# Kernel tuning notes

Hardware: AMD Instinct MI355X
Metric: run time of the kernel (lower is better)

The kernel has to match this reference:

```python
import jax, jax.numpy as jnp
import numpy as np

N = 100000
E = 1_600_000
IN_CH = 64
HID = 32       # per-head hidden dim
HEADS = 4
OUT_CH = 6
NEG_SLOPE = 0.2


def _glorot(key, shape):
    fan_in, fan_out = shape[0], shape[-1]
    lim = jnp.sqrt(6.0 / (fan_in + fan_out))
    return jax.random.uniform(key, shape, jnp.float32, -lim, lim)


def setup_inputs() -> dict:
    key = jax.random.key(0)
    ks = jax.random.split(key, 20)
    x = jax.random.normal(ks[0], (N, IN_CH), jnp.float32)
    edge_index = jax.random.randint(ks[1], (2, E), 0, N, jnp.int64)
    batch = jnp.zeros((N,), jnp.int64)
    inp = {"x": x, "edge_index": edge_index, "batch": batch}
    inp["W0"] = _glorot(ks[2], (IN_CH, HEADS * HID))
    inp["as0"] = _glorot(ks[3], (HEADS, HID))
    inp["ad0"] = _glorot(ks[4], (HEADS, HID))
    inp["b0"] = jnp.zeros((HEADS * HID,), jnp.float32)
    inp["W1"] = _glorot(ks[5], (HEADS * HID, HEADS * HID))
    inp["as1"] = _glorot(ks[6], (HEADS, HID))
    inp["ad1"] = _glorot(ks[7], (HEADS, HID))
    inp["b1"] = jnp.zeros((HEADS * HID,), jnp.float32)
    inp["W2"] = _glorot(ks[8], (HEADS * HID, HEADS * HID))
    inp["as2"] = _glorot(ks[9], (HEADS, HID))
    inp["ad2"] = _glorot(ks[10], (HEADS, HID))
    inp["b2"] = jnp.zeros((HEADS * HID,), jnp.float32)
    # final layer: 128 -> 6, 1 head, no concat (mean)
    inp["W3"] = _glorot(ks[11], (HEADS * HID, OUT_CH))
    inp["as3"] = _glorot(ks[12], (1, OUT_CH))
    inp["ad3"] = _glorot(ks[13], (1, OUT_CH))
    inp["b3"] = jnp.zeros((OUT_CH,), jnp.float32)
    return inp


def gat_conv(x, src, dst, W, a_src, a_dst, b, heads, concat):
    """PyG GATConv: linear -> per-edge attention -> segment softmax over dst -> scatter-add."""
    n = x.shape[0]
    h = (x @ W).reshape(n, heads, -1)                       # [N,H,D]
    al_s = jnp.sum(h * a_src, axis=-1)                      # [N,H]
    al_d = jnp.sum(h * a_dst, axis=-1)                      # [N,H]
    e = jax.nn.leaky_relu(al_s[src] + al_d[dst], NEG_SLOPE)  # [E,H]
    m = jax.ops.segment_max(e, dst, num_segments=n)         # segment softmax (stable)
    ex = jnp.exp(e - m[dst])
    s = jax.ops.segment_sum(ex, dst, num_segments=n)
    alpha = ex / (s[dst] + 1e-16)                           # [E,H]
    out = jax.ops.segment_sum(alpha[:, :, None] * h[src], dst, num_segments=n)  # [N,H,D]
    out = out.reshape(n, -1) if concat else out.mean(axis=1)
    return out + b


def reference(x, edge_index, batch, W0, as0, ad0, b0, W1, as1, ad1, b1,
              W2, as2, ad2, b2, W3, as3, ad3, b3):
    n = x.shape[0]
    # PyG GATConv adds self-loops by default; edge set is static (no pooling), add once.
    ar = jnp.arange(n, dtype=edge_index.dtype)
    ei = jnp.concatenate([edge_index, jnp.stack([ar, ar])], axis=1)
    src, dst = ei[0], ei[1]
    x = jax.nn.elu(gat_conv(x, src, dst, W0, as0, ad0, b0, HEADS, True))
    x = jax.nn.elu(gat_conv(x, src, dst, W1, as1, ad1, b1, HEADS, True))
    x = jax.nn.elu(gat_conv(x, src, dst, W2, as2, ad2, b2, HEADS, True))
    x = gat_conv(x, src, dst, W3, as3, ad3, b3, 1, False)   # final layer: no activation
    return x
```

## Files before the change

### kernel.cpp

```cpp
#include <hip/hip_runtime.h>
#include <hip/hip_bf16.h>
#include <hip/hip_fp16.h>

#define IN_CH 64
#define HID 32
#define HEADS 4
#define OUT_CH 6
#define NEG_SLOPE 0.2f

typedef __attribute__((ext_vector_type(8))) _Float16 half8;
typedef __attribute__((ext_vector_type(4))) float f32x4;


#define PBLK 256
#define CAP 6144

__global__ __launch_bounds__(256) void part_count(const int* __restrict__ ei, int E, int EN,
                                                  int NB, int epb, int* __restrict__ counts) {
    __shared__ int cnt[512];
    int b = blockIdx.x, t = threadIdx.x;
    for (int i = t; i < NB; i += 256) cnt[i] = 0;
    __syncthreads();
    int e0 = b * epb;
    int e1 = min(e0 + epb, EN);
    for (int e = e0 + t; e < e1; e += 256) {
        int d = (e < E) ? ei[E + e] : (e - E);
        atomicAdd(&cnt[d >> 8], 1);
    }
    __syncthreads();
    for (int i = t; i < NB; i += 256) counts[(size_t)i * PBLK + b] = cnt[i];
}

__global__ __launch_bounds__(256) void bucket_tot(const int* __restrict__ counts,
                                                  int* __restrict__ btot) {
    __shared__ int red[256];
    int k = blockIdx.x, t = threadIdx.x;
    red[t] = counts[(size_t)k * PBLK + t];
    __syncthreads();
    for (int off = 128; off; off >>= 1) {
        if (t < off) red[t] += red[t + off];
        __syncthreads();
    }
    if (t == 0) btot[k] = red[0];
}

__global__ __launch_bounds__(256) void bucket_scan(const int* __restrict__ btot, int NB, int EN,
                                                   int* __restrict__ bstart) {
    __shared__ int tmp[256];
    int t = threadIdx.x;
    int chunk = (NB + 255) >> 8;
    int s0 = t * chunk, s1 = min(s0 + chunk, NB);
    int sum = 0;
    for (int i = s0; i < s1; ++i) sum += btot[i];
    tmp[t] = sum;
    __syncthreads();
    for (int off = 1; off < 256; off <<= 1) {
        int v = (t >= off) ? tmp[t - off] : 0;
        __syncthreads();
        tmp[t] += v;
        __syncthreads();
    }
    int run = (t == 0) ? 0 : tmp[t - 1];
    for (int i = s0; i < s1; ++i) {
        int c = btot[i];
        bstart[i] = run;
        run += c;
    }
    if (t == 255) bstart[NB] = EN;
}

__global__ __launch_bounds__(256) void bucket_base(int* __restrict__ counts,
                                                   const int* __restrict__ bstart) {
    __shared__ int sc[256];
    int k = blockIdx.x, t = threadIdx.x;
    int v = counts[(size_t)k * PBLK + t];
    sc[t] = v;
    __syncthreads();
    for (int off = 1; off < 256; off <<= 1) {
        int u = (t >= off) ? sc[t - off] : 0;
        __syncthreads();
        sc[t] += u;
        __syncthreads();
    }
    counts[(size_t)k * PBLK + t] = bstart[k] + sc[t] - v;
}

__global__ __launch_bounds__(256) void part_scatter(const int* __restrict__ ei, int E, int EN,
                                                    int NB, int epb,
                                                    const int* __restrict__ base,
                                                    int2* __restrict__ ebuf) {
    __shared__ int cur[512];
    int b = blockIdx.x, t = threadIdx.x;
    for (int i = t; i < NB; i += 256) cur[i] = base[(size_t)i * PBLK + b];
    __syncthreads();
    int e0 = b * epb;
    int e1 = min(e0 + epb, EN);
    for (int e = e0 + t; e < e1; e += 256) {
        int s, d;
        if (e < E) { s = ei[e]; d = ei[E + e]; }
        else       { s = e - E; d = s; }
        int slot = atomicAdd(&cur[d >> 8], 1);
        ebuf[slot] = make_int2(s, d & 255);
    }
}

__global__ __launch_bounds__(256) void bucket_csr(const int2* __restrict__ ebuf,
                                                  const int* __restrict__ bstart,
                                                  int NB, int N, int EN,
                                                  int* __restrict__ row_start,
                                                  int* __restrict__ csr_src) {
    __shared__ int cnt[256];
    __shared__ int sc[256];
    __shared__ int stage[CAP];
    int k = blockIdx.x, t = threadIdx.x;
    int s0 = bstart[k], s1 = bstart[k + 1];
    int len = s1 - s0;
    cnt[t] = 0;
    __syncthreads();
    for (int i = t; i < len; i += 256) atomicAdd(&cnt[ebuf[s0 + i].y], 1);
    __syncthreads();
    int v = cnt[t];
    sc[t] = v;
    __syncthreads();
    for (int off = 1; off < 256; off <<= 1) {
        int u = (t >= off) ? sc[t - off] : 0;
        __syncthreads();
        sc[t] += u;
        __syncthreads();
    }
    int excl = sc[t] - v;
    int g = (k << 8) + t;
    if (g < N) row_start[g] = s0 + excl;
    if (k == NB - 1 && t == 0) row_start[N] = EN;
    bool fits = (len <= CAP);
    cnt[t] = fits ? excl : s0 + excl;
    __syncthreads();
    if (fits) {
        for (int i = t; i < len; i += 256) {
            int2 e = ebuf[s0 + i];
            int slot = atomicAdd(&cnt[e.y], 1);
            stage[slot] = e.x;
        }
        __syncthreads();
        for (int i = t; i < len; i += 256) csr_src[s0 + i] = stage[i];
    } else {
        for (int i = t; i < len; i += 256) {
            int2 e = ebuf[s0 + i];
            int slot = atomicAdd(&cnt[e.y], 1);
            csr_src[slot] = e.x;
        }
    }
}


__global__ void xconv_kernel(const float* __restrict__ x, __half* __restrict__ xh, int total4) {
    int t = blockIdx.x * blockDim.x + threadIdx.x;
    if (t >= total4) return;
    float4 v = *reinterpret_cast<const float4*>(x + (size_t)t * 4);
    __half2* op = reinterpret_cast<__half2*>(xh + (size_t)t * 4);
    op[0] = __float22half2_rn(make_float2(v.x, v.y));
    op[1] = __float22half2_rn(make_float2(v.z, v.w));
}

__global__ void wtrans_kernel(const float* __restrict__ W, __half* __restrict__ WT,
                              int K, int kshift) {
    int o = blockIdx.x * blockDim.x + threadIdx.x;
    if (o >= (K << 7)) return;
    int c = o >> kshift;
    int k = o & (K - 1);
    WT[o] = __float2half(W[(size_t)k * 128 + c]);
}


__global__ __launch_bounds__(256) void gemm_mfma(const __half* __restrict__ A,
                                                 const __half* __restrict__ WT,
                                                 const float* __restrict__ avs,
                                                 const float* __restrict__ avd,
                                                 __half* __restrict__ C,
                                                 float* __restrict__ als,
                                                 float* __restrict__ ald,
                                                 int N, int K) {
    int tid = threadIdx.x;
    int wv = tid >> 6, lane = tid & 63;
    int row0 = blockIdx.x * 64 + wv * 16;
    int lrow = lane & 15;
    int lk = (lane >> 4) * 8;
    int garow = row0 + lrow;

    half8 afrag[4];
#pragma unroll
    for (int ks = 0; ks < 4; ++ks) {
        half8 z = {(_Float16)0, (_Float16)0, (_Float16)0, (_Float16)0,
                   (_Float16)0, (_Float16)0, (_Float16)0, (_Float16)0};
        afrag[ks] = z;
    }
    if (garow < N) {
        const __half* ap = A + (size_t)garow * K + lk;
        if (K == 128) {
#pragma unroll
            for (int ks = 0; ks < 4; ++ks)
                afrag[ks] = *reinterpret_cast<const half8*>(ap + ks * 32);
        } else {
#pragma unroll
            for (int ks = 0; ks < 2; ++ks)
                afrag[ks] = *reinterpret_cast<const half8*>(ap + ks * 32);
        }
    }

    f32x4 acc[8];
#pragma unroll
    for (int t = 0; t < 8; ++t) acc[t] = (f32x4){0.f, 0.f, 0.f, 0.f};

#pragma unroll
    for (int t = 0; t < 8; ++t) {
        const __half* wb = WT + (size_t)(t * 16 + lrow) * K + lk;
        if (K == 128) {
#pragma unroll
            for (int ks = 0; ks < 4; ++ks) {
                half8 bfrag = *reinterpret_cast<const half8*>(wb + ks * 32);
                acc[t] = __builtin_amdgcn_mfma_f32_16x16x32_f16(afrag[ks], bfrag, acc[t], 0, 0, 0);
            }
        } else {
#pragma unroll
            for (int ks = 0; ks < 2; ++ks) {
                half8 bfrag = *reinterpret_cast<const half8*>(wb + ks * 32);
                acc[t] = __builtin_amdgcn_mfma_f32_16x16x32_f16(afrag[ks], bfrag, acc[t], 0, 0, 0);
            }
        }
    }

    int rbase = (lane >> 4) * 4;
#pragma unroll
    for (int t = 0; t < 8; ++t) {
#pragma unroll
        for (int j = 0; j < 4; ++j) {
            int gr = row0 + rbase + j;
            if (gr < N) C[(size_t)gr * 128 + t * 16 + lrow] = __float2half(acc[t][j]);
        }
    }
    float ps[4][4], pd[4][4];
#pragma unroll
    for (int h = 0; h < 4; ++h)
#pragma unroll
        for (int j = 0; j < 4; ++j) { ps[h][j] = 0.f; pd[h][j] = 0.f; }
#pragma unroll
    for (int t = 0; t < 8; ++t) {
        int ht = t >> 1;
        float as_c = avs[t * 16 + lrow];
        float ad_c = avd[t * 16 + lrow];
#pragma unroll
        for (int j = 0; j < 4; ++j) {
            ps[ht][j] += acc[t][j] * as_c;
            pd[ht][j] += acc[t][j] * ad_c;
        }
    }
#pragma unroll
    for (int h = 0; h < 4; ++h) {
#pragma unroll
        for (int j = 0; j < 4; ++j) {
            float s = ps[h][j], d = pd[h][j];
            s += __shfl_xor(s, 1); d += __shfl_xor(d, 1);
            s += __shfl_xor(s, 2); d += __shfl_xor(d, 2);
            s += __shfl_xor(s, 4); d += __shfl_xor(d, 4);
            s += __shfl_xor(s, 8); d += __shfl_xor(d, 8);
            if (lrow == 0) {
                int gr = row0 + rbase + j;
                if (gr < N) {
                    als[(size_t)gr * 4 + h] = s;
                    ald[(size_t)gr * 4 + h] = d;
                }
            }
        }
    }
}


__device__ __forceinline__ float lrelu(float x) { return x > 0.f ? x : NEG_SLOPE * x; }

__global__ __launch_bounds__(256) void agg_kernel(const __half* __restrict__ h,
                                                  const float* __restrict__ als4,
                                                  const float* __restrict__ ald4,
                                                  const int* __restrict__ row_start,
                                                  const int* __restrict__ csr_src,
                                                  const float* __restrict__ bias,
                                                  __half* __restrict__ xout,
                                                  int N, int applyElu) {
    int v = (int)((blockIdx.x * blockDim.x + threadIdx.x) >> 6);
    int lane = threadIdx.x & 63;
    if (v >= N) return;
    int base = row_start[v], end = row_start[v + 1];

    int half_ = lane >> 5;
    int dim4 = (lane & 31) * 4;
    int hd2  = (lane & 31) >> 3;

    float aldh = ald4[(size_t)v * 4 + hd2];
    float alsh = als4[(size_t)v * 4 + hd2];
    float em = lrelu(alsh + aldh);
    const __half* hdim = h + dim4;
    const float* alsb = als4 + hd2;

    float4 acc  = make_float4(0.f, 0.f, 0.f, 0.f);
    float4 acc2 = make_float4(0.f, 0.f, 0.f, 0.f);
    float ssum = 0.f, ssum2 = 0.f;

    int j = base + half_;
    for (; j + 6 < end; j += 8) {
        int s0 = csr_src[j + 0];
        int s1 = csr_src[j + 2];
        int s2 = csr_src[j + 4];
        int s3 = csr_src[j + 6];
        float a0 = alsb[(size_t)s0 * 4];
        float a1 = alsb[(size_t)s1 * 4];
        float a2 = alsb[(size_t)s2 * 4];
        float a3 = alsb[(size_t)s3 * 4];
        uint2 r0 = *reinterpret_cast<const uint2*>(hdim + (size_t)s0 * 128);
        uint2 r1 = *reinterpret_cast<const uint2*>(hdim + (size_t)s1 * 128);
        uint2 r2 = *reinterpret_cast<const uint2*>(hdim + (size_t)s2 * 128);
        uint2 r3 = *reinterpret_cast<const uint2*>(hdim + (size_t)s3 * 128);
        float e0 = __expf(lrelu(a0 + aldh) - em);
        float e1 = __expf(lrelu(a1 + aldh) - em);
        float e2 = __expf(lrelu(a2 + aldh) - em);
        float e3 = __expf(lrelu(a3 + aldh) - em);
        ssum  += e0 + e2;
        ssum2 += e1 + e3;
        float2 f0a = __half22float2(*reinterpret_cast<__half2*>(&r0.x));
        float2 f0b = __half22float2(*reinterpret_cast<__half2*>(&r0.y));
        float2 f1a = __half22float2(*reinterpret_cast<__half2*>(&r1.x));
        float2 f1b = __half22float2(*reinterpret_cast<__half2*>(&r1.y));
        float2 f2a = __half22float2(*reinterpret_cast<__half2*>(&r2.x));
        float2 f2b = __half22float2(*reinterpret_cast<__half2*>(&r2.y));
        float2 f3a = __half22float2(*reinterpret_cast<__half2*>(&r3.x));
        float2 f3b = __half22float2(*reinterpret_cast<__half2*>(&r3.y));
        acc.x  += e0 * f0a.x; acc.y  += e0 * f0a.y; acc.z  += e0 * f0b.x; acc.w  += e0 * f0b.y;
        acc2.x += e1 * f1a.x; acc2.y += e1 * f1a.y; acc2.z += e1 * f1b.x; acc2.w += e1 * f1b.y;
        acc.x  += e2 * f2a.x; acc.y  += e2 * f2a.y; acc.z  += e2 * f2b.x; acc.w  += e2 * f2b.y;
        acc2.x += e3 * f3a.x; acc2.y += e3 * f3a.y; acc2.z += e3 * f3b.x; acc2.w += e3 * f3b.y;
    }
    for (; j < end; j += 2) {
        int s0 = csr_src[j];
        float a0 = alsb[(size_t)s0 * 4];
        uint2 r0 = *reinterpret_cast<const uint2*>(hdim + (size_t)s0 * 128);
        float e0 = __expf(lrelu(a0 + aldh) - em);
        ssum += e0;
        float2 f0a = __half22float2(*reinterpret_cast<__half2*>(&r0.x));
        float2 f0b = __half22float2(*reinterpret_cast<__half2*>(&r0.y));
        acc.x += e0 * f0a.x; acc.y += e0 * f0a.y; acc.z += e0 * f0b.x; acc.w += e0 * f0b.y;
    }
    acc.x += acc2.x; acc.y += acc2.y; acc.z += acc2.z; acc.w += acc2.w;
    ssum += ssum2;
    acc.x += __shfl_xor(acc.x, 32);
    acc.y += __shfl_xor(acc.y, 32);
    acc.z += __shfl_xor(acc.z, 32);
    acc.w += __shfl_xor(acc.w, 32);
    ssum  += __shfl_xor(ssum, 32);

    if (lane < 32) {
        float inv = 1.0f / (ssum + 1e-16f);
        float4 bv = *reinterpret_cast<const float4*>(bias + dim4);
        float4 o;
        o.x = acc.x * inv + bv.x;
        o.y = acc.y * inv + bv.y;
        o.z = acc.z * inv + bv.z;
        o.w = acc.w * inv + bv.w;
        if (applyElu) {
            o.x = o.x > 0.f ? o.x : expm1f(o.x);
            o.y = o.y > 0.f ? o.y : expm1f(o.y);
            o.z = o.z > 0.f ? o.z : expm1f(o.z);
            o.w = o.w > 0.f ? o.w : expm1f(o.w);
        }
        __half2* op = reinterpret_cast<__half2*>(xout + (size_t)v * 128 + dim4);
        op[0] = __float22half2_rn(make_float2(o.x, o.y));
        op[1] = __float22half2_rn(make_float2(o.z, o.w));
    }
}


__global__ void gemm3_kernel(const __half* __restrict__ x, const float* __restrict__ W,
                             const float* __restrict__ as3, const float* __restrict__ ad3,
                             float* __restrict__ h3, float* __restrict__ als3,
                             float* __restrict__ ald3, int N) {
    int n = blockIdx.x * blockDim.x + threadIdx.x;
    if (n >= N) return;
    float acc[6] = {0.f, 0.f, 0.f, 0.f, 0.f, 0.f};
    const __half* xp = x + (size_t)n * 128;
#pragma unroll 2
    for (int k8 = 0; k8 < 16; ++k8) {
        uint4 rv = *reinterpret_cast<const uint4*>(xp + k8 * 8);
        float2 fa = __half22float2(*reinterpret_cast<__half2*>(&rv.x));
        float2 fb = __half22float2(*reinterpret_cast<__half2*>(&rv.y));
        float2 fc = __half22float2(*reinterpret_cast<__half2*>(&rv.z));
        float2 fd = __half22float2(*reinterpret_cast<__half2*>(&rv.w));
        float xv[8] = {fa.x, fa.y, fb.x, fb.y, fc.x, fc.y, fd.x, fd.y};
        const float* w0 = W + (size_t)(k8 * 8) * 6;
#pragma unroll
        for (int kk = 0; kk < 8; ++kk)
#pragma unroll
            for (int q = 0; q < 6; ++q)
                acc[q] += xv[kk] * w0[kk * 6 + q];
    }
    float s = 0.f, d = 0.f;
#pragma unroll
    for (int q = 0; q < 6; ++q) {
        s += acc[q] * as3[q];
        d += acc[q] * ad3[q];
        h3[(size_t)n * 6 + q] = acc[q];
    }
    als3[n] = s;
    ald3[n] = d;
}

__global__ void agg3_kernel(const float* __restrict__ h3, const float* __restrict__ als3,
                            const float* __restrict__ ald3, const int* __restrict__ row_start,
                            const int* __restrict__ csr_src, const float* __restrict__ b3,
                            float* __restrict__ out, int N) {
    int v = blockIdx.x * blockDim.x + threadIdx.x;
    if (v >= N) return;
    int base = row_start[v], end = row_start[v + 1];
    float aldv = ald3[v];
    float em = lrelu(als3[v] + aldv);
    float ssum = 0.f;
    float acc[6] = {0.f, 0.f, 0.f, 0.f, 0.f, 0.f};
    float acc2[6] = {0.f, 0.f, 0.f, 0.f, 0.f, 0.f};
    int j = base;
    for (; j + 1 < end; j += 2) {
        int sa = csr_src[j], sb = csr_src[j + 1];
        float ea = __expf(lrelu(als3[sa] + aldv) - em);
        float eb = __expf(lrelu(als3[sb] + aldv) - em);
        ssum += ea + eb;
        const float* ha = h3 + (size_t)sa * 6;
        const float* hb = h3 + (size_t)sb * 6;
#pragma unroll
        for (int q = 0; q < 6; ++q) acc[q] += ea * ha[q];
#pragma unroll
        for (int q = 0; q < 6; ++q) acc2[q] += eb * hb[q];
    }
    if (j < end) {
        int sa = csr_src[j];
        float ea = __expf(lrelu(als3[sa] + aldv) - em);
        ssum += ea;
        const float* ha = h3 + (size_t)sa * 6;
#pragma unroll
        for (int q = 0; q < 6; ++q) acc[q] += ea * ha[q];
    }
    float inv = 1.f / (ssum + 1e-16f);
#pragma unroll
    for (int q = 0; q < 6; ++q) out[(size_t)v * 6 + q] = (acc[q] + acc2[q]) * inv + b3[q];
}


extern "C" void kernel_launch(void* const* d_in, const int* in_sizes, int n_in,
                              void* d_out, int out_size, void* d_ws, size_t ws_size,
                              hipStream_t stream) {
    const float* x    = (const float*)d_in[0];
    const int*   ei   = (const int*)d_in[1];
    const float* W0   = (const float*)d_in[3];
    const float* as0  = (const float*)d_in[4];
    const float* ad0  = (const float*)d_in[5];
    const float* b0   = (const float*)d_in[6];
    const float* W1   = (const float*)d_in[7];
    const float* as1  = (const float*)d_in[8];
    const float* ad1  = (const float*)d_in[9];
    const float* b1   = (const float*)d_in[10];
    const float* W2   = (const float*)d_in[11];
    const float* as2  = (const float*)d_in[12];
    const float* ad2  = (const float*)d_in[13];
    const float* b2   = (const float*)d_in[14];
    const float* W3   = (const float*)d_in[15];
    const float* as3  = (const float*)d_in[16];
    const float* ad3  = (const float*)d_in[17];
    const float* b3   = (const float*)d_in[18];
    float* out = (float*)d_out;

    int N = in_sizes[0] / IN_CH;
    int E = in_sizes[1] / 2;
    int EN = E + N;
    int NB = (N + 255) >> 8;
    int epb = (EN + PBLK - 1) / PBLK;

    char* p = (char*)d_ws;
    auto alloc = [&](size_t bytes) {
        char* q = p;
        p += (bytes + 255) & ~(size_t)255;
        return q;
    };
    __half* xh   = (__half*)alloc((size_t)N * 64 * 2);
    __half* hbuf = (__half*)alloc((size_t)N * 128 * 2);
    __half* xA   = (__half*)alloc((size_t)N * 128 * 2);
    __half* xB   = (__half*)alloc((size_t)N * 128 * 2);
    __half* WT0  = (__half*)alloc((size_t)128 * 64 * 2);
    __half* WT1  = (__half*)alloc((size_t)128 * 128 * 2);
    __half* WT2  = (__half*)alloc((size_t)128 * 128 * 2);
    float* als  = (float*)alloc((size_t)N * 4 * 4);
    float* ald  = (float*)alloc((size_t)N * 4 * 4);
    float* h3   = (float*)alloc((size_t)N * 6 * 4);
    float* als3 = (float*)alloc((size_t)N * 4);
    float* ald3 = (float*)alloc((size_t)N * 4);
    int* row_start = (int*)alloc((size_t)(N + 1) * 4);
    int* csr_src   = (int*)alloc((size_t)EN * 4);
    int2* ebuf     = (int2*)alloc((size_t)EN * 8);
    int* counts    = (int*)alloc((size_t)NB * PBLK * 4);
    int* btot      = (int*)alloc((size_t)NB * 4);
    int* bstart    = (int*)alloc((size_t)(NB + 1) * 4);
    (void)ws_size; (void)n_in; (void)out_size;

    part_count<<<PBLK, 256, 0, stream>>>(ei, E, EN, NB, epb, counts);
    bucket_tot<<<NB, 256, 0, stream>>>(counts, btot);
    bucket_scan<<<1, 256, 0, stream>>>(btot, NB, EN, bstart);
    bucket_base<<<NB, 256, 0, stream>>>(counts, bstart);
    part_scatter<<<PBLK, 256, 0, stream>>>(ei, E, EN, NB, epb, counts, ebuf);
    bucket_csr<<<NB, 256, 0, stream>>>(ebuf, bstart, NB, N, EN, row_start, csr_src);

    xconv_kernel<<<(N * 16 + 255) / 256, 256, 0, stream>>>(x, xh, N * 16);
    wtrans_kernel<<<(128 * 64 + 255) / 256, 256, 0, stream>>>(W0, WT0, 64, 6);
    wtrans_kernel<<<(128 * 128 + 255) / 256, 256, 0, stream>>>(W1, WT1, 128, 7);
    wtrans_kernel<<<(128 * 128 + 255) / 256, 256, 0, stream>>>(W2, WT2, 128, 7);

    int gemm_grid = (N + 63) / 64;
    int agg_grid  = (N + 3) / 4;
    int n_grid    = (N + 255) / 256;

    gemm_mfma<<<gemm_grid, 256, 0, stream>>>(xh, WT0, as0, ad0, hbuf, als, ald, N, 64);
    agg_kernel<<<agg_grid, 256, 0, stream>>>(hbuf, als, ald, row_start, csr_src, b0, xA, N, 1);

    gemm_mfma<<<gemm_grid, 256, 0, stream>>>(xA, WT1, as1, ad1, hbuf, als, ald, N, 128);
    agg_kernel<<<agg_grid, 256, 0, stream>>>(hbuf, als, ald, row_start, csr_src, b1, xB, N, 1);

    gemm_mfma<<<gemm_grid, 256, 0, stream>>>(xB, WT2, as2, ad2, hbuf, als, ald, N, 128);
    agg_kernel<<<agg_grid, 256, 0, stream>>>(hbuf, als, ald, row_start, csr_src, b2, xA, N, 1);

    gemm3_kernel<<<n_grid, 256, 0, stream>>>(xA, W3, as3, ad3, h3, als3, ald3, N);
    agg3_kernel<<<n_grid, 256, 0, stream>>>(h3, als3, ald3, row_start, csr_src, b3, out, N);
}
```

Measured before the change: 445.8 us.

## Compute edge softmax weights once per chunk in LDS; fuse input fp16 conversion into GEMM

The aggregation kernel now processes each node's edges in chunks of 64. In each chunk every lane loads one source index and all four heads' attention logits as a float4, computes the four exp weights and stages them with the source index in shared memory. The gather loop then reads those staged values, so the redundant per-head exp and logit loads that each lane group used to repeat are removed. The first-layer GEMM now reads the fp32 input directly and converts it in registers, which eliminates the separate xconv pass and its buffer. The staging adds LDS traffic and wave barriers per chunk, and the half-to-float conversions now go through unions.

```diff
diff --git a/kernel.cpp b/kernel.cpp
--- a/kernel.cpp
+++ b/kernel.cpp
@@ -153,15 +153,6 @@
 }
 
 
-__global__ void xconv_kernel(const float* __restrict__ x, __half* __restrict__ xh, int total4) {
-    int t = blockIdx.x * blockDim.x + threadIdx.x;
-    if (t >= total4) return;
-    float4 v = *reinterpret_cast<const float4*>(x + (size_t)t * 4);
-    __half2* op = reinterpret_cast<__half2*>(xh + (size_t)t * 4);
-    op[0] = __float22half2_rn(make_float2(v.x, v.y));
-    op[1] = __float22half2_rn(make_float2(v.z, v.w));
-}
-
 __global__ void wtrans_kernel(const float* __restrict__ W, __half* __restrict__ WT,
                               int K, int kshift) {
     int o = blockIdx.x * blockDim.x + threadIdx.x;
@@ -173,6 +164,7 @@
 
 
 __global__ __launch_bounds__(256) void gemm_mfma(const __half* __restrict__ A,
+                                                 const float* __restrict__ Af,
                                                  const __half* __restrict__ WT,
                                                  const float* __restrict__ avs,
                                                  const float* __restrict__ avd,
@@ -195,15 +187,21 @@
         afrag[ks] = z;
     }
     if (garow < N) {
-        const __half* ap = A + (size_t)garow * K + lk;
         if (K == 128) {
+            const __half* ap = A + (size_t)garow * 128 + lk;
 #pragma unroll
             for (int ks = 0; ks < 4; ++ks)
                 afrag[ks] = *reinterpret_cast<const half8*>(ap + ks * 32);
         } else {
-#pragma unroll
-            for (int ks = 0; ks < 2; ++ks)
-                afrag[ks] = *reinterpret_cast<const half8*>(ap + ks * 32);
+            const float* ap = Af + (size_t)garow * 64 + lk;
+#pragma unroll
+            for (int ks = 0; ks < 2; ++ks) {
+                float4 f0 = *reinterpret_cast<const float4*>(ap + ks * 32);
+                float4 f1 = *reinterpret_cast<const float4*>(ap + ks * 32 + 4);
+                half8 fr = {(_Float16)f0.x, (_Float16)f0.y, (_Float16)f0.z, (_Float16)f0.w,
+                            (_Float16)f1.x, (_Float16)f1.y, (_Float16)f1.z, (_Float16)f1.w};
+                afrag[ks] = fr;
+            }
         }
     }
 
@@ -285,7 +283,10 @@
                                                   const float* __restrict__ bias,
                                                   __half* __restrict__ xout,
                                                   int N, int applyElu) {
-    int v = (int)((blockIdx.x * blockDim.x + threadIdx.x) >> 6);
+    __shared__ float ex_s[4][256];
+    __shared__ int   so_s[4][64];
+    int w = threadIdx.x >> 6;
+    int v = blockIdx.x * 4 + w;
     int lane = threadIdx.x & 63;
     if (v >= N) return;
     int base = row_start[v], end = row_start[v + 1];
@@ -294,68 +295,83 @@
     int dim4 = (lane & 31) * 4;
     int hd2  = (lane & 31) >> 3;
 
-    float aldh = ald4[(size_t)v * 4 + hd2];
-    float alsh = als4[(size_t)v * 4 + hd2];
-    float em = lrelu(alsh + aldh);
+    float4 aldv = *reinterpret_cast<const float4*>(ald4 + (size_t)v * 4);
+    float4 alsv = *reinterpret_cast<const float4*>(als4 + (size_t)v * 4);
+    float4 em4;
+    em4.x = lrelu(alsv.x + aldv.x);
+    em4.y = lrelu(alsv.y + aldv.y);
+    em4.z = lrelu(alsv.z + aldv.z);
+    em4.w = lrelu(alsv.w + aldv.w);
+
     const __half* hdim = h + dim4;
-    const float* alsb = als4 + hd2;
-
+    float4 sum4 = make_float4(0.f, 0.f, 0.f, 0.f);
     float4 acc  = make_float4(0.f, 0.f, 0.f, 0.f);
     float4 acc2 = make_float4(0.f, 0.f, 0.f, 0.f);
-    float ssum = 0.f, ssum2 = 0.f;
-
-    int j = base + half_;
-    for (; j + 6 < end; j += 8) {
-        int s0 = csr_src[j + 0];
-        int s1 = csr_src[j + 2];
-        int s2 = csr_src[j + 4];
-        int s3 = csr_src[j + 6];
-        float a0 = alsb[(size_t)s0 * 4];
-        float a1 = alsb[(size_t)s1 * 4];
-        float a2 = alsb[(size_t)s2 * 4];
-        float a3 = alsb[(size_t)s3 * 4];
-        uint2 r0 = *reinterpret_cast<const uint2*>(hdim + (size_t)s0 * 128);
-        uint2 r1 = *reinterpret_cast<const uint2*>(hdim + (size_t)s1 * 128);
-        uint2 r2 = *reinterpret_cast<const uint2*>(hdim + (size_t)s2 * 128);
-        uint2 r3 = *reinterpret_cast<const uint2*>(hdim + (size_t)s3 * 128);
-        float e0 = __expf(lrelu(a0 + aldh) - em);
-        float e1 = __expf(lrelu(a1 + aldh) - em);
-        float e2 = __expf(lrelu(a2 + aldh) - em);
-        float e3 = __expf(lrelu(a3 + aldh) - em);
-        ssum  += e0 + e2;
-        ssum2 += e1 + e3;
-        float2 f0a = __half22float2(*reinterpret_cast<__half2*>(&r0.x));
-        float2 f0b = __half22float2(*reinterpret_cast<__half2*>(&r0.y));
-        float2 f1a = __half22float2(*reinterpret_cast<__half2*>(&r1.x));
-        float2 f1b = __half22float2(*reinterpret_cast<__half2*>(&r1.y));
-        float2 f2a = __half22float2(*reinterpret_cast<__half2*>(&r2.x));
-        float2 f2b = __half22float2(*reinterpret_cast<__half2*>(&r2.y));
-        float2 f3a = __half22float2(*reinterpret_cast<__half2*>(&r3.x));
-        float2 f3b = __half22float2(*reinterpret_cast<__half2*>(&r3.y));
-        acc.x  += e0 * f0a.x; acc.y  += e0 * f0a.y; acc.z  += e0 * f0b.x; acc.w  += e0 * f0b.y;
-        acc2.x += e1 * f1a.x; acc2.y += e1 * f1a.y; acc2.z += e1 * f1b.x; acc2.w += e1 * f1b.y;
-        acc.x  += e2 * f2a.x; acc.y  += e2 * f2a.y; acc.z  += e2 * f2b.x; acc.w  += e2 * f2b.y;
-        acc2.x += e3 * f3a.x; acc2.y += e3 * f3a.y; acc2.z += e3 * f3b.x; acc2.w += e3 * f3b.y;
-    }
-    for (; j < end; j += 2) {
-        int s0 = csr_src[j];
-        float a0 = alsb[(size_t)s0 * 4];
-        uint2 r0 = *reinterpret_cast<const uint2*>(hdim + (size_t)s0 * 128);
-        float e0 = __expf(lrelu(a0 + aldh) - em);
-        ssum += e0;
-        float2 f0a = __half22float2(*reinterpret_cast<__half2*>(&r0.x));
-        float2 f0b = __half22float2(*reinterpret_cast<__half2*>(&r0.y));
-        acc.x += e0 * f0a.x; acc.y += e0 * f0a.y; acc.z += e0 * f0b.x; acc.w += e0 * f0b.y;
+
+    for (int c = base; c < end; c += 64) {
+        int j = c + lane;
+        bool valid = j < end;
+        int s = valid ? csr_src[j] : 0;
+        float4 ex4 = make_float4(0.f, 0.f, 0.f, 0.f);
+        if (valid) {
+            float4 a = *reinterpret_cast<const float4*>(als4 + (size_t)s * 4);
+            ex4.x = __expf(lrelu(a.x + aldv.x) - em4.x);
+            ex4.y = __expf(lrelu(a.y + aldv.y) - em4.y);
+            ex4.z = __expf(lrelu(a.z + aldv.z) - em4.z);
+            ex4.w = __expf(lrelu(a.w + aldv.w) - em4.w);
+            sum4.x += ex4.x; sum4.y += ex4.y; sum4.z += ex4.z; sum4.w += ex4.w;
+        }
+        *reinterpret_cast<float4*>(&ex_s[w][lane * 4]) = ex4;
+        so_s[w][lane] = s;
+        __builtin_amdgcn_wave_barrier();
+        asm volatile("" ::: "memory");
+
+        int cnt = end - c; if (cnt > 64) cnt = 64;
+        int t = half_;
+        for (; t + 6 < cnt; t += 8) {
+            int i0 = t, i1 = t + 2, i2 = t + 4, i3 = t + 6;
+            int s0 = so_s[w][i0], s1 = so_s[w][i1], s2 = so_s[w][i2], s3 = so_s[w][i3];
+            float e0 = ex_s[w][i0 * 4 + hd2], e1 = ex_s[w][i1 * 4 + hd2];
+            float e2 = ex_s[w][i2 * 4 + hd2], e3 = ex_s[w][i3 * 4 + hd2];
+            union { uint2 u; __half hh[4]; } r0, r1, r2, r3;
+            r0.u = *reinterpret_cast<const uint2*>(hdim + (size_t)s0 * 128);
+            r1.u = *reinterpret_cast<const uint2*>(hdim + (size_t)s1 * 128);
+            r2.u = *reinterpret_cast<const uint2*>(hdim + (size_t)s2 * 128);
+            r3.u = *reinterpret_cast<const uint2*>(hdim + (size_t)s3 * 128);
+            acc.x  += e0 * (float)r0.hh[0]; acc.y  += e0 * (float)r0.hh[1];
+            acc.z  += e0 * (float)r0.hh[2]; acc.w  += e0 * (float)r0.hh[3];
+            acc2.x += e1 * (float)r1.hh[0]; acc2.y += e1 * (float)r1.hh[1];
+            acc2.z += e1 * (float)r1.hh[2]; acc2.w += e1 * (float)r1.hh[3];
+            acc.x  += e2 * (float)r2.hh[0]; acc.y  += e2 * (float)r2.hh[1];
+            acc.z  += e2 * (float)r2.hh[2]; acc.w  += e2 * (float)r2.hh[3];
+            acc2.x += e3 * (float)r3.hh[0]; acc2.y += e3 * (float)r3.hh[1];
+            acc2.z += e3 * (float)r3.hh[2]; acc2.w += e3 * (float)r3.hh[3];
+        }
+        for (; t < cnt; t += 2) {
+            int s0 = so_s[w][t];
+            float e0 = ex_s[w][t * 4 + hd2];
+            union { uint2 u; __half hh[4]; } r0;
+            r0.u = *reinterpret_cast<const uint2*>(hdim + (size_t)s0 * 128);
+            acc.x += e0 * (float)r0.hh[0]; acc.y += e0 * (float)r0.hh[1];
+            acc.z += e0 * (float)r0.hh[2]; acc.w += e0 * (float)r0.hh[3];
+        }
+        __builtin_amdgcn_wave_barrier();
+        asm volatile("" ::: "memory");
     }
     acc.x += acc2.x; acc.y += acc2.y; acc.z += acc2.z; acc.w += acc2.w;
-    ssum += ssum2;
     acc.x += __shfl_xor(acc.x, 32);
     acc.y += __shfl_xor(acc.y, 32);
     acc.z += __shfl_xor(acc.z, 32);
     acc.w += __shfl_xor(acc.w, 32);
-    ssum  += __shfl_xor(ssum, 32);
-
+#pragma unroll
+    for (int off = 32; off; off >>= 1) {
+        sum4.x += __shfl_xor(sum4.x, off);
+        sum4.y += __shfl_xor(sum4.y, off);
+        sum4.z += __shfl_xor(sum4.z, off);
+        sum4.w += __shfl_xor(sum4.w, off);
+    }
     if (lane < 32) {
+        float ssum = (hd2 == 0) ? sum4.x : (hd2 == 1) ? sum4.y : (hd2 == 2) ? sum4.z : sum4.w;
         float inv = 1.0f / (ssum + 1e-16f);
         float4 bv = *reinterpret_cast<const float4*>(bias + dim4);
         float4 o;
@@ -386,18 +402,16 @@
     const __half* xp = x + (size_t)n * 128;
 #pragma unroll 2
     for (int k8 = 0; k8 < 16; ++k8) {
-        uint4 rv = *reinterpret_cast<const uint4*>(xp + k8 * 8);
-        float2 fa = __half22float2(*reinterpret_cast<__half2*>(&rv.x));
-        float2 fb = __half22float2(*reinterpret_cast<__half2*>(&rv.y));
-        float2 fc = __half22float2(*reinterpret_cast<__half2*>(&rv.z));
-        float2 fd = __half22float2(*reinterpret_cast<__half2*>(&rv.w));
-        float xv[8] = {fa.x, fa.y, fb.x, fb.y, fc.x, fc.y, fd.x, fd.y};
+        union { uint4 u; __half hh[8]; } rv;
+        rv.u = *reinterpret_cast<const uint4*>(xp + k8 * 8);
         const float* w0 = W + (size_t)(k8 * 8) * 6;
 #pragma unroll
-        for (int kk = 0; kk < 8; ++kk)
+        for (int kk = 0; kk < 8; ++kk) {
+            float xv = (float)rv.hh[kk];
 #pragma unroll
             for (int q = 0; q < 6; ++q)
-                acc[q] += xv[kk] * w0[kk * 6 + q];
+                acc[q] += xv * w0[kk * 6 + q];
+        }
     }
     float s = 0.f, d = 0.f;
 #pragma unroll
@@ -484,7 +498,6 @@
         p += (bytes + 255) & ~(size_t)255;
         return q;
     };
-    __half* xh   = (__half*)alloc((size_t)N * 64 * 2);
     __half* hbuf = (__half*)alloc((size_t)N * 128 * 2);
     __half* xA   = (__half*)alloc((size_t)N * 128 * 2);
     __half* xB   = (__half*)alloc((size_t)N * 128 * 2);
@@ -511,7 +524,6 @@
     part_scatter<<<PBLK, 256, 0, stream>>>(ei, E, EN, NB, epb, counts, ebuf);
     bucket_csr<<<NB, 256, 0, stream>>>(ebuf, bstart, NB, N, EN, row_start, csr_src);
 
-    xconv_kernel<<<(N * 16 + 255) / 256, 256, 0, stream>>>(x, xh, N * 16);
     wtrans_kernel<<<(128 * 64 + 255) / 256, 256, 0, stream>>>(W0, WT0, 64, 6);
     wtrans_kernel<<<(128 * 128 + 255) / 256, 256, 0, stream>>>(W1, WT1, 128, 7);
     wtrans_kernel<<<(128 * 128 + 255) / 256, 256, 0, stream>>>(W2, WT2, 128, 7);
@@ -520,13 +532,13 @@
     int agg_grid  = (N + 3) / 4;
     int n_grid    = (N + 255) / 256;
 
-    gemm_mfma<<<gemm_grid, 256, 0, stream>>>(xh, WT0, as0, ad0, hbuf, als, ald, N, 64);
+    gemm_mfma<<<gemm_grid, 256, 0, stream>>>(nullptr, x, WT0, as0, ad0, hbuf, als, ald, N, 64);
     agg_kernel<<<agg_grid, 256, 0, stream>>>(hbuf, als, ald, row_start, csr_src, b0, xA, N, 1);
 
-    gemm_mfma<<<gemm_grid, 256, 0, stream>>>(xA, WT1, as1, ad1, hbuf, als, ald, N, 128);
+    gemm_mfma<<<gemm_grid, 256, 0, stream>>>(xA, nullptr, WT1, as1, ad1, hbuf, als, ald, N, 128);
     agg_kernel<<<agg_grid, 256, 0, stream>>>(hbuf, als, ald, row_start, csr_src, b1, xB, N, 1);
 
-    gemm_mfma<<<gemm_grid, 256, 0, stream>>>(xB, WT2, as2, ad2, hbuf, als, ald, N, 128);
+    gemm_mfma<<<gemm_grid, 256, 0, stream>>>(xB, nullptr, WT2, as2, ad2, hbuf, als, ald, N, 128);
     agg_kernel<<<agg_grid, 256, 0, stream>>>(hbuf, als, ald, row_start, csr_src, b2, xA, N, 1);
 
     gemm3_kernel<<<n_grid, 256, 0, stream>>>(xA, W3, as3, ad3, h3, als3, ald3, N);
```

Result: no change. 454.7 us (+2.0%).
